# Performance work log

Hardware: AMD Instinct MI355X
Metric: run time of the kernel (lower is better)

The kernel has to match this reference:

```python
import jax, jax.numpy as jnp
from jax import lax
import numpy as np

L = 21                      # total_labels (incl. background class 0)
VARIANCES = (0.1, 0.1, 0.2, 0.2)
NMS_THRESHOLD = 0.5
MAX_TOTAL_SIZE = 200        # also max_output_size_per_class
SCORE_THRESHOLD = 0.5


def setup_inputs() -> dict:
    key = jax.random.key(0)
    k1, k2, k3, k4 = jax.random.split(key, 4)
    B, N = 1, 2048
    # valid normalized rois: y1<y2, x1<x2, inside [0,1]
    yx = jax.random.uniform(k1, (B, N, 2)) * 0.8
    hw = jax.random.uniform(k2, (B, N, 2)) * 0.19 + 0.01
    roi_bboxes = jnp.concatenate([yx, yx + hw], axis=-1)
    pred_deltas = jax.random.normal(k3, (B, N, L * 4)) * 0.2
    pred_label_probs = jax.random.uniform(k4, (B, N, L))
    return {"roi_bboxes": roi_bboxes, "pred_deltas": pred_deltas,
            "pred_label_probs": pred_label_probs}


def _decode(rois, deltas):
    # rois/deltas: (..., 4), boxes [y1,x1,y2,x2], deltas [dy,dx,dh,dw]
    h = rois[..., 2] - rois[..., 0]
    w = rois[..., 3] - rois[..., 1]
    cy = rois[..., 0] + 0.5 * h
    cx = rois[..., 1] + 0.5 * w
    nh = jnp.exp(deltas[..., 2]) * h
    nw = jnp.exp(deltas[..., 3]) * w
    ncy = deltas[..., 0] * h + cy
    ncx = deltas[..., 1] * w + cx
    return jnp.stack([ncy - 0.5 * nh, ncx - 0.5 * nw,
                      ncy + 0.5 * nh, ncx + 0.5 * nw], axis=-1)


def _iou_matrix(b):  # b: (N,4) -> (N,N)
    y1, x1, y2, x2 = b[:, 0], b[:, 1], b[:, 2], b[:, 3]
    area = (y2 - y1) * (x2 - x1)
    ih = jnp.clip(jnp.minimum(y2[:, None], y2[None, :]) - jnp.maximum(y1[:, None], y1[None, :]), 0.0)
    iw = jnp.clip(jnp.minimum(x2[:, None], x2[None, :]) - jnp.maximum(x1[:, None], x1[None, :]), 0.0)
    inter = ih * iw
    return inter / (area[:, None] + area[None, :] - inter + 1e-9)


def _nms_sorted(boxes, scores):
    # greedy per-class NMS; returns boxes/scores sorted by score desc + keep mask
    order = jnp.argsort(-scores)
    b = boxes[order]
    s = scores[order]
    iou = _iou_matrix(lax.stop_gradient(b))  # NMS decisions are non-differentiable
    n = b.shape[0]
    idx = jnp.arange(n)

    def body(i, keep):
        sup = keep[i] & (iou[i] > NMS_THRESHOLD) & (idx > i)
        return keep & jnp.logical_not(sup)

    keep = lax.fori_loop(0, n, body, jnp.ones((n,), bool))
    keep = keep & (jnp.cumsum(keep) <= MAX_TOTAL_SIZE)  # max_output_size_per_class
    return b, s, keep


def reference(roi_bboxes, pred_deltas, pred_label_probs):
    B, N, _ = roi_bboxes.shape  # B == 1 (module's slicing logic assumes it)
    deltas = pred_deltas.reshape(B, N, L, 4) * jnp.asarray(VARIANCES, pred_deltas.dtype)
    rois = jnp.broadcast_to(roi_bboxes[:, :, None, :], (B, N, L, 4))
    boxes = _decode(rois, deltas)  # (B,N,L,4)

    # zero out all class scores for rois whose argmax is background (class 0)
    am = jnp.argmax(pred_label_probs, axis=-1)
    scores = jnp.where((am != 0)[..., None], pred_label_probs, 0.0)

    boxes_c = jnp.transpose(boxes[0], (1, 0, 2))  # (L,N,4)
    scores_c = scores[0].T                         # (L,N)
    b_s, s_s, keep = jax.vmap(_nms_sorted)(boxes_c, scores_c)

    cls = jnp.broadcast_to(jnp.arange(L, dtype=s_s.dtype)[:, None], (L, N))
    flat_b = b_s.reshape(-1, 4)
    flat_s = s_s.reshape(-1)
    flat_c = cls.reshape(-1)

    def select(kmask):
        sc = jnp.where(kmask.reshape(-1), flat_s, -1.0)
        top_sc, top_idx = lax.top_k(sc, MAX_TOTAL_SIZE)
        return top_sc, jnp.clip(flat_b[top_idx], 0.0, 1.0), flat_c[top_idx]

    # thresholded combined NMS result (padded with zeros, like TF CNMS)
    sc_t, b_t, l_t = select(keep & (s_s > SCORE_THRESHOLD))
    valid_t = sc_t > SCORE_THRESHOLD
    out_b = jnp.where(valid_t[:, None], b_t, 0.0)
    out_s = jnp.where(valid_t, sc_t, 0.0)
    out_l = jnp.where(valid_t, l_t, 0.0)

    # fallback: no detections above threshold -> best unthresholded detection
    sc_u, b_u, l_u = select(keep)
    best = sc_u[0]
    have = best >= 0.001
    slot0 = jnp.arange(MAX_TOTAL_SIZE) == 0
    fb_b = jnp.where((slot0 & have)[:, None], b_u[0], 0.0)
    fb_s = jnp.where(slot0 & have, best, 0.0)
    fb_l = jnp.where(slot0 & have, l_u[0], 0.0)

    use_fb = jnp.sum(valid_t) == 0
    fin_b = jnp.where(use_fb, fb_b, out_b)[None]  # (1, MAX_TOTAL_SIZE, 4)
    fin_s = jnp.where(use_fb, fb_s, out_s)[None]  # (1, MAX_TOTAL_SIZE)
    fin_l = jnp.where(use_fb, fb_l, out_l)[None]  # (1, MAX_TOTAL_SIZE)
    return fin_b, fin_l, fin_s
```

## Files before the change

### kernel.cpp

```cpp
#include <hip/hip_runtime.h>
#include <stdint.h>

#define NN 2048
#define LL 21
#define CAP 200
#define TOT (LL * CAP)
#define TMAX 320
#define NCH (TMAX / 64)
#define NBK 1024
#define ARRCAP 1200

typedef unsigned long long u64;
typedef unsigned int u32;

__device__ __forceinline__ u64 shfl_u64(u64 v, int lane) {
    int lo = (int)(u32)(v & 0xFFFFFFFFull);
    int hi = (int)(u32)(v >> 32);
    lo = __shfl(lo, lane);
    hi = __shfl(hi, lane);
    return ((u64)(u32)hi << 32) | (u32)lo;
}

__device__ __forceinline__ u64 shfl_xor_u64(u64 v, int mask) {
    int lo = (int)(u32)(v & 0xFFFFFFFFull);
    int hi = (int)(u32)(v >> 32);
    lo = __shfl_xor(lo, mask);
    hi = __shfl_xor(hi, mask);
    return ((u64)(u32)hi << 32) | (u32)lo;
}

__device__ __forceinline__ float4 clip01(float4 b) {
    b.x = fminf(fmaxf(b.x, 0.0f), 1.0f);
    b.y = fminf(fmaxf(b.y, 0.0f), 1.0f);
    b.z = fminf(fmaxf(b.z, 0.0f), 1.0f);
    b.w = fminf(fmaxf(b.w, 0.0f), 1.0f);
    return b;
}

__device__ __forceinline__ float4 decode_box(const float4 roi, const float4 dd) {
#pragma clang fp contract(off)
    float h  = roi.z - roi.x;
    float w  = roi.w - roi.y;
    float cy = roi.x + 0.5f * h;
    float cx = roi.y + 0.5f * w;
    float d0 = dd.x * 0.1f;
    float d1 = dd.y * 0.1f;
    float d2 = dd.z * 0.2f;
    float d3 = dd.w * 0.2f;
    float nh = (float)exp((double)d2) * h;
    float nw = (float)exp((double)d3) * w;
    float ncy = d0 * h + cy;
    float ncx = d1 * w + cx;
    return make_float4(ncy - 0.5f * nh, ncx - 0.5f * nw, ncy + 0.5f * nh, ncx + 0.5f * nw);
}

__device__ __forceinline__ bool iou_gt(const float4 a, const float4 b) {
#pragma clang fp contract(off)
    float areaA = (a.z - a.x) * (a.w - a.y);
    float areaB = (b.z - b.x) * (b.w - b.y);
    float ih = fminf(a.z, b.z) - fmaxf(a.x, b.x);
    ih = fmaxf(ih, 0.0f);
    float iw = fminf(a.w, b.w) - fmaxf(a.y, b.y);
    iw = fmaxf(iw, 0.0f);
    float inter = ih * iw;
    float denom = ((areaA + areaB) - inter) + 1e-9f;
    return (inter / denom) > 0.5f;
}

__device__ __forceinline__ int rb_of(u64 key) {
    u32 sb = (u32)(key >> 32);
    int rb = 1023 - (int)((sb - 0x3F000000u) >> 13);
    return min(max(rb, 0), 1023);
}

__device__ __forceinline__ u64 lowmask(int n) {
    return (n >= 64) ? ~0ull : ((1ull << n) - 1ull);
}

__device__ __forceinline__ void desc_scan(int* histR, int* dstart, int* cursor,
                                          int* wtot, int t, int nthr) {
    const int PB = NBK / nthr;
    const int lane = t & 63, w = t >> 6;
    int c[4], local = 0;
    for (int k = 0; k < PB; ++k) { c[k] = histR[PB * t + k]; local += c[k]; }
    int incl = local;
    for (int d = 1; d < 64; d <<= 1) {
        int v = __shfl_up(incl, d);
        if (lane >= d) incl += v;
    }
    if (lane == 63) wtot[w] = incl;
    __syncthreads();
    int woff = 0;
    for (int i = 0; i < w; ++i) woff += wtot[i];
    int run = woff + incl - local;
    for (int k = 0; k < PB; ++k) {
        dstart[PB * t + k] = run;
        cursor[PB * t + k] = run;
        run += c[k];
    }
    __syncthreads();
}

__global__ __launch_bounds__(256) void score_kernel(
    const float* __restrict__ probs,
    u32* __restrict__ scoreT)
{
    __shared__ float tile[256 * LL];
    const int a0 = blockIdx.x * 256;
    const int t = threadIdx.x;
    const float4* src = (const float4*)probs + blockIdx.x * 1344;
    float4* dst = (float4*)tile;
    for (int i = t; i < 1344; i += 256) dst[i] = src[i];
    __syncthreads();
    const float* row = tile + t * LL;
    float best = row[0];
    int bi = 0;
    for (int j = 1; j < LL; ++j) {
        float v = row[j];
        if (v > best) { best = v; bi = j; }
    }
    for (int c = 0; c < LL; ++c)
        scoreT[c * NN + a0 + t] = (bi != 0) ? __float_as_uint(row[c]) : 0u;
}

#define SMEM_B 45056
#define NBASE 16384

__global__ __launch_bounds__(512) void per_class_kernel(
    const u32* __restrict__ scoreT,
    const float* __restrict__ roi,
    const float* __restrict__ deltas,
    u64* __restrict__ cand_key,
    float4* __restrict__ cand_box,
    u64* __restrict__ fb_key,
    float4* __restrict__ fb_box)
{
    const int cls = blockIdx.x;
    const int t = threadIdx.x;
    const int lane = t & 63;

    __shared__ char sm[SMEM_B];
    __shared__ int sCnt, sK;
    __shared__ u64 sGmax;
    __shared__ u64 keepm[NCH];
    __shared__ int wtot[8];

    u64* skey  = (u64*)sm;
    u64* skey3 = (u64*)sm;
    u64* skey2 = (u64*)(sm + NBASE);
    int* histR  = (int*)(sm + 32768);
    int* cursor = (int*)(sm + 36864);
    int* dstart = (int*)(sm + 40960);

    if (t == 0) { sCnt = 0; sK = 0; sGmax = 0ull; }
    for (int s = t; s < CAP; s += 512) cand_key[cls * CAP + s] = 0ull;
    for (int i = t; i < NBK; i += 512) histR[i] = 0;
    __syncthreads();

    uint4 s4 = ((const uint4*)(scoreT + cls * NN))[t];
    u32 sv[4] = { s4.x, s4.y, s4.z, s4.w };
    u64 lq[4];
    int ln = 0;
    u64 lmax = 0ull;
    for (int k = 0; k < 4; ++k) {
        u32 a = 4 * t + k;
        u64 key = ((u64)sv[k] << 32) | (u32)(~a);
        if (key > lmax) lmax = key;
        if (sv[k] > 0x3F000000u) lq[ln++] = key;
    }
    for (int d = 1; d < 64; d <<= 1) {
        u64 o = shfl_xor_u64(lmax, d);
        if (o > lmax) lmax = o;
    }
    if (lane == 0) atomicMax(&sGmax, lmax);
    int incl = ln;
    for (int d = 1; d < 64; d <<= 1) {
        int v = __shfl_up(incl, d);
        if (lane >= d) incl += v;
    }
    int wsum = __shfl(incl, 63);
    int wbase = 0;
    if (lane == 63) wbase = atomicAdd(&sCnt, wsum);
    wbase = __shfl(wbase, 63);
    int off = wbase + incl - ln;
    for (int j = 0; j < ln; ++j) skey[off + j] = lq[j];
    __syncthreads();
    const int M = sCnt;

    if (t == 0) {
        u64 g = sGmax;
        u32 a0 = ~(u32)(g & 0xFFFFFFFFull);
        float4 rb = *(const float4*)(roi + a0 * 4);
        float4 dd = *(const float4*)(deltas + a0 * (LL * 4) + cls * 4);
        fb_box[cls] = decode_box(rb, dd);
        fb_key[cls] = (g & 0xFFFFFFFF00000000ull) | (u32)(~(u32)(cls * NN));
    }

    for (int i = t; i < M; i += 512) atomicAdd(&histR[rb_of(skey[i])], 1);
    __syncthreads();
    desc_scan(histR, dstart, cursor, wtot, t, 512);
    for (int i = t; i < M; i += 512) {
        u64 k = skey[i];
        int pos = atomicAdd(&cursor[rb_of(k)], 1);
        skey2[pos] = k;
    }
    __syncthreads();
    for (int p = t; p < M; p += 512) {
        u64 k = skey2[p];
        int rb = rb_of(k);
        int s = dstart[rb], e = s + histR[rb];
        int rnk = s;
        for (int q = s; q < e; ++q) rnk += (skey2[q] > k) ? 1 : 0;
        skey3[rnk] = k;
    }
    __syncthreads();

    float4* cbox = (float4*)(sm + NBASE);
    u64* R  = (u64*)(sm + NBASE + 5120);
    u64* Tm = (u64*)(sm + NBASE + 7680);
    float4* kept = (float4*)(sm + NBASE + 12800);

    const int TT = min(M, TMAX);
    const int NCHe = (TT + 63) / 64;
    const int NJ = NCHe * (NCHe + 1) / 2;

    for (int r = t; r < TT; r += 512) {
        u32 a = ~(u32)(skey3[r] & 0xFFFFFFFFull);
        float4 rbx = *(const float4*)(roi + a * 4);
        float4 dd = *(const float4*)(deltas + a * (LL * 4) + cls * 4);
        cbox[r] = decode_box(rbx, dd);
    }
    __syncthreads();

    for (int task = t; task < NJ * 64; task += 512) {
        const int jobid = task >> 6, j = task & 63;
        int cj = 0, acc = 0;
        while (acc + cj + 1 <= jobid) { acc += cj + 1; ++cj; }
        const int ci = jobid - acc;
        const int gj = cj * 64 + j;
        const int nbj = min(64, TT - cj * 64);
        if (ci == cj) {
            u64 row = 0ull;
            if (j < nbj) {
                float4 bj = cbox[gj];
                for (int r2 = j + 1; r2 < nbj; ++r2)
                    if (iou_gt(bj, cbox[cj * 64 + r2])) row |= (1ull << r2);
            }
            R[cj * 64 + j] = row;
        } else {
            u64 wd = 0ull;
            if (j < nbj) {
                float4 bj = cbox[gj];
                const float4* cb = cbox + ci * 64;
                for (int i = 0; i < 64; ++i)
                    if (iou_gt(cb[i], bj)) wd |= (1ull << i);
            }
            Tm[(cj * (cj - 1) / 2 + ci) * 64 + j] = wd;
        }
    }
    __syncthreads();

    if (t < 64) {
        int K = 0;
        for (int cj = 0; cj < NCHe; ++cj) {
            if (K >= CAP) break;
            const int nb = min(64, TT - cj * 64);
            u64 row = R[cj * 64 + t];
            bool ext = (t >= nb);
            for (int ci = 0; ci < cj; ++ci)
                if (Tm[(cj * (cj - 1) / 2 + ci) * 64 + t] & keepm[ci]) ext = true;
            u64 rem = __ballot(ext);
            const u64 nz = __ballot(row != 0ull) & ~rem;
            u64 m = nz;
            while (m) {
                int i = __ffsll(m) - 1;
                u64 ri = shfl_u64(row, i);
                rem |= ri;
                u64 gt = (i == 63) ? 0ull : ~lowmask(i + 1);
                m = nz & ~rem & gt;
            }
            u64 keep = ~rem & lowmask(nb);
            if (t == 0) keepm[cj] = keep;
            if (t < nb && ((keep >> t) & 1ull)) {
                int krank = K + __popcll(keep & lowmask(t));
                if (krank < CAP) {
                    kept[krank] = cbox[cj * 64 + t];
                    int slot = cls * CAP + krank;
                    cand_key[slot] = (skey3[cj * 64 + t] & 0xFFFFFFFF00000000ull) |
                                     (u32)(~(u32)slot);
                    cand_box[slot] = cbox[cj * 64 + t];
                }
            }
            K += __popcll(keep);
        }
        if (t == 0) sK = K;
    }
    __syncthreads();

    int K = sK;
    if (K < CAP && M > TT) {
        u64* sup = (u64*)(sm + NBASE + 5120);
        unsigned char* extq = (unsigned char*)(sm + NBASE + 9216);
        const int g = t >> 6, r = t & 63;
        for (int base = TT; base < M; base += 64) {
            K = sK;
            if (K >= CAP) break;
            const int nb = min(64, M - base);
            if (t < nb) {
                u32 a = ~(u32)(skey3[base + t] & 0xFFFFFFFFull);
                float4 rbx = *(const float4*)(roi + a * 4);
                float4 dd = *(const float4*)(deltas + a * (LL * 4) + cls * 4);
                cbox[t] = decode_box(rbx, dd);
            }
            __syncthreads();
            u64 bits = 0ull;
            if (r < nb) {
                float4 br = cbox[r];
                int lo = max(r + 1, g * 8), hi = min(nb, (g + 1) * 8);
                for (int r2 = lo; r2 < hi; ++r2)
                    if (iou_gt(br, cbox[r2])) bits |= (1ull << r2);
            }
            sup[g * 64 + r] = bits;
            bool f = false;
            if (r < nb) {
                float4 bm = cbox[r];
                int per = (K + 7) >> 3;
                int e0 = g * per, e1 = min(K, e0 + per);
                for (int e = e0; e < e1; ++e)
                    if (iou_gt(kept[e], bm)) { f = true; break; }
            }
            extq[g * 64 + r] = f ? 1 : 0;
            __syncthreads();
            if (t < 64) {
                u64 row = 0ull;
                int extv = 0;
                for (int j = 0; j < 8; ++j) { row |= sup[j * 64 + t]; extv |= extq[j * 64 + t]; }
                bool ext = (t < nb) ? (extv != 0) : true;
                u64 rem = __ballot(ext);
                const u64 nz = __ballot(row != 0ull) & ~rem;
                u64 m = nz;
                while (m) {
                    int i = __ffsll(m) - 1;
                    u64 ri = shfl_u64(row, i);
                    rem |= ri;
                    u64 gt = (i == 63) ? 0ull : ~lowmask(i + 1);
                    m = nz & ~rem & gt;
                }
                u64 keep = ~rem & lowmask(nb);
                if (t < nb && ((keep >> t) & 1ull)) {
                    int krank = K + __popcll(keep & lowmask(t));
                    if (krank < CAP) {
                        kept[krank] = cbox[t];
                        int slot = cls * CAP + krank;
                        cand_key[slot] = (skey3[base + t] & 0xFFFFFFFF00000000ull) |
                                         (u32)(~(u32)slot);
                        cand_box[slot] = cbox[t];
                    }
                }
                if (t == 0) sK = K + __popcll(keep);
            }
            __syncthreads();
        }
    }
}

__global__ __launch_bounds__(256) void topk_kernel(
    const u64* __restrict__ cand_key,
    const float4* __restrict__ cand_box,
    const u64* __restrict__ fb_key,
    const float4* __restrict__ fb_box,
    float* __restrict__ out)
{
    const int t = threadIdx.x;
    __shared__ u64 keys[TOT];
    __shared__ int histR[NBK], cursor[NBK], dstart[NBK];
    __shared__ u64 arr[ARRCAP];
    __shared__ u64 outk[CAP];
    __shared__ int wtot[8];
    __shared__ int sRbstar;

    for (int i = t; i < NBK; i += 256) histR[i] = 0;
    for (int i = t; i < CAP; i += 256) outk[i] = 0ull;
    if (t == 0) sRbstar = NBK - 1;
    __syncthreads();

    const ulong2* ck2 = (const ulong2*)cand_key;
    for (int i = t; i < TOT / 2; i += 256) {
        ulong2 k2 = ck2[i];
        keys[2 * i]     = k2.x;
        keys[2 * i + 1] = k2.y;
        if (k2.x != 0ull) atomicAdd(&histR[rb_of(k2.x)], 1);
        if (k2.y != 0ull) atomicAdd(&histR[rb_of(k2.y)], 1);
    }
    __syncthreads();
    desc_scan(histR, dstart, cursor, wtot, t, 256);
    for (int k = 0; k < 4; ++k) {
        int rb = 4 * t + k;
        if (dstart[rb] < CAP && dstart[rb] + histR[rb] >= CAP) sRbstar = rb;
    }
    __syncthreads();
    const int rbstar = sRbstar;

    for (int i = t; i < TOT; i += 256) {
        u64 k = keys[i];
        if (k != 0ull) {
            int rb = rb_of(k);
            if (rb <= rbstar) {
                int pos = atomicAdd(&cursor[rb], 1);
                if (pos < ARRCAP) arr[pos] = k;
            }
        }
    }
    __syncthreads();

    const int E = min(dstart[rbstar] + histR[rbstar], ARRCAP);
    for (int p = t; p < E; p += 256) {
        u64 k = arr[p];
        int rb = rb_of(k);
        int s = dstart[rb], e = min(s + histR[rb], ARRCAP);
        int rnk = s;
        for (int q = s; q < e; ++q) rnk += (arr[q] > k) ? 1 : 0;
        if (rnk < CAP) outk[rnk] = k;
    }
    __syncthreads();

    for (int o = t; o < CAP; o += 256) {
        u64 key = outk[o];
        float4 b = make_float4(0.0f, 0.0f, 0.0f, 0.0f);
        float lab = 0.0f, sc = 0.0f;
        if (key != 0ull) {
            u32 slot = ~(u32)(key & 0xFFFFFFFFull);
            sc = __uint_as_float((u32)(key >> 32));
            lab = (float)(slot / CAP);
            b = clip01(cand_box[slot]);
        }
        out[o * 4 + 0] = b.x;
        out[o * 4 + 1] = b.y;
        out[o * 4 + 2] = b.z;
        out[o * 4 + 3] = b.w;
        out[4 * CAP + o] = lab;
        out[5 * CAP + o] = sc;
    }
    __syncthreads();

    if (t == 0 && outk[0] == 0ull) {
        u64 best = 0ull;
        int bc = 0;
        for (int c = 0; c < LL; ++c) {
            u64 k = fb_key[c];
            if (k > best) { best = k; bc = c; }
        }
        float bs = __uint_as_float((u32)(best >> 32));
        if (bs >= 0.001f) {
            float4 bb = clip01(fb_box[bc]);
            out[0] = bb.x; out[1] = bb.y; out[2] = bb.z; out[3] = bb.w;
            out[4 * CAP] = (float)bc;
            out[5 * CAP] = bs;
        }
    }
}

extern "C" void kernel_launch(void* const* d_in, const int* in_sizes, int n_in,
                              void* d_out, int out_size, void* d_ws, size_t ws_size,
                              hipStream_t stream) {
    const float* roi    = (const float*)d_in[0];
    const float* deltas = (const float*)d_in[1];
    const float* probs  = (const float*)d_in[2];
    float* out = (float*)d_out;

    char* ws = (char*)d_ws;
    u32*    scoreT   = (u32*)ws;
    u64*    cand_key = (u64*)(ws + 172032);
    float4* cand_box = (float4*)(ws + 205632);
    u64*    fb_key   = (u64*)(ws + 272832);
    float4* fb_box   = (float4*)(ws + 273008);

    score_kernel<<<NN / 256, 256, 0, stream>>>(probs, scoreT);
    per_class_kernel<<<LL, 512, 0, stream>>>(scoreT, roi, deltas,
                                             cand_key, cand_box, fb_key, fb_box);
    topk_kernel<<<1, 256, 0, stream>>>(cand_key, cand_box, fb_key, fb_box, out);
}
```

Measured before the change: 93.66 us.

## Fuse top-k into per-class kernel via last-block counter and precompute box areas

Drops the separate top-k launch: each per-class block increments a global counter once it finishes, and the last block to finish runs the cross-class top-k merge using 512 threads. The change also folds the histogram build into the key scatter and decodes candidate boxes inside the rank loop, removing two barriers. Box areas are computed once and stored in shared memory so the IoU loops do not recompute them. In exchange it adds a memset launch, atomics and fences, and more shared memory per block. The merge work is now serialised behind the slowest class block.

```diff
diff --git a/kernel.cpp b/kernel.cpp
--- a/kernel.cpp
+++ b/kernel.cpp
@@ -54,6 +54,11 @@
     return make_float4(ncy - 0.5f * nh, ncx - 0.5f * nw, ncy + 0.5f * nh, ncx + 0.5f * nw);
 }
 
+__device__ __forceinline__ float area_of(const float4 b) {
+#pragma clang fp contract(off)
+    return (b.z - b.x) * (b.w - b.y);
+}
+
 __device__ __forceinline__ bool iou_gt(const float4 a, const float4 b) {
 #pragma clang fp contract(off)
     float areaA = (a.z - a.x) * (a.w - a.y);
@@ -67,6 +72,18 @@
     return (inter / denom) > 0.5f;
 }
 
+__device__ __forceinline__ bool iou_gt_pre(const float4 a, const float4 b,
+                                           float areaA, float areaB) {
+#pragma clang fp contract(off)
+    float ih = fminf(a.z, b.z) - fmaxf(a.x, b.x);
+    ih = fmaxf(ih, 0.0f);
+    float iw = fminf(a.w, b.w) - fmaxf(a.y, b.y);
+    iw = fmaxf(iw, 0.0f);
+    float inter = ih * iw;
+    float denom = ((areaA + areaB) - inter) + 1e-9f;
+    return (inter / denom) > 0.5f;
+}
+
 __device__ __forceinline__ int rb_of(u64 key) {
     u32 sb = (u32)(key >> 32);
     int rb = 1023 - (int)((sb - 0x3F000000u) >> 13);
@@ -123,8 +140,11 @@
         scoreT[c * NN + a0 + t] = (bi != 0) ? __float_as_uint(row[c]) : 0u;
 }
 
-#define SMEM_B 45056
-#define NBASE 16384
+#define SMEM_B 64384
+#define A1OFF 17408
+#define A2OFF 34816
+#define A3OFF 47104
+#define A4OFF 63104
 
 __global__ __launch_bounds__(512) void per_class_kernel(
     const u32* __restrict__ scoreT,
@@ -133,24 +153,31 @@
     u64* __restrict__ cand_key,
     float4* __restrict__ cand_box,
     u64* __restrict__ fb_key,
-    float4* __restrict__ fb_box)
+    float4* __restrict__ fb_box,
+    int* __restrict__ ctr,
+    float* __restrict__ out)
 {
     const int cls = blockIdx.x;
     const int t = threadIdx.x;
     const int lane = t & 63;
 
     __shared__ char sm[SMEM_B];
-    __shared__ int sCnt, sK;
+    __shared__ int sCnt, sK, sLast, sRbstar;
     __shared__ u64 sGmax;
     __shared__ u64 keepm[NCH];
     __shared__ int wtot[8];
 
     u64* skey  = (u64*)sm;
     u64* skey3 = (u64*)sm;
-    u64* skey2 = (u64*)(sm + NBASE);
-    int* histR  = (int*)(sm + 32768);
-    int* cursor = (int*)(sm + 36864);
-    int* dstart = (int*)(sm + 40960);
+    u64* skey2 = (u64*)(sm + A1OFF);
+    int* histR  = (int*)(sm + A2OFF);
+    int* cursor = (int*)(sm + A2OFF + 4096);
+    int* dstart = (int*)(sm + A2OFF + 8192);
+    float4* cbox = (float4*)(sm + A3OFF);
+    u64* R  = (u64*)(sm + A3OFF + 5120);
+    u64* Tm = (u64*)(sm + A3OFF + 7680);
+    float4* kept = (float4*)(sm + A3OFF + 12800);
+    float* area = (float*)(sm + A4OFF);
 
     if (t == 0) { sCnt = 0; sK = 0; sGmax = 0ull; }
     for (int s = t; s < CAP; s += 512) cand_key[cls * CAP + s] = 0ull;
@@ -183,9 +210,13 @@
     if (lane == 63) wbase = atomicAdd(&sCnt, wsum);
     wbase = __shfl(wbase, 63);
     int off = wbase + incl - ln;
-    for (int j = 0; j < ln; ++j) skey[off + j] = lq[j];
+    for (int j = 0; j < ln; ++j) {
+        skey[off + j] = lq[j];
+        atomicAdd(&histR[rb_of(lq[j])], 1);
+    }
     __syncthreads();
     const int M = sCnt;
+    const int TT = min(M, TMAX);
 
     if (t == 0) {
         u64 g = sGmax;
@@ -196,15 +227,15 @@
         fb_key[cls] = (g & 0xFFFFFFFF00000000ull) | (u32)(~(u32)(cls * NN));
     }
 
-    for (int i = t; i < M; i += 512) atomicAdd(&histR[rb_of(skey[i])], 1);
-    __syncthreads();
     desc_scan(histR, dstart, cursor, wtot, t, 512);
+
     for (int i = t; i < M; i += 512) {
         u64 k = skey[i];
         int pos = atomicAdd(&cursor[rb_of(k)], 1);
         skey2[pos] = k;
     }
     __syncthreads();
+
     for (int p = t; p < M; p += 512) {
         u64 k = skey2[p];
         int rb = rb_of(k);
@@ -212,25 +243,19 @@
         int rnk = s;
         for (int q = s; q < e; ++q) rnk += (skey2[q] > k) ? 1 : 0;
         skey3[rnk] = k;
-    }
-    __syncthreads();
-
-    float4* cbox = (float4*)(sm + NBASE);
-    u64* R  = (u64*)(sm + NBASE + 5120);
-    u64* Tm = (u64*)(sm + NBASE + 7680);
-    float4* kept = (float4*)(sm + NBASE + 12800);
-
-    const int TT = min(M, TMAX);
+        if (rnk < TT) {
+            u32 a = ~(u32)(k & 0xFFFFFFFFull);
+            float4 rbx = *(const float4*)(roi + a * 4);
+            float4 dd = *(const float4*)(deltas + a * (LL * 4) + cls * 4);
+            float4 bx = decode_box(rbx, dd);
+            cbox[rnk] = bx;
+            area[rnk] = area_of(bx);
+        }
+    }
+    __syncthreads();
+
     const int NCHe = (TT + 63) / 64;
     const int NJ = NCHe * (NCHe + 1) / 2;
-
-    for (int r = t; r < TT; r += 512) {
-        u32 a = ~(u32)(skey3[r] & 0xFFFFFFFFull);
-        float4 rbx = *(const float4*)(roi + a * 4);
-        float4 dd = *(const float4*)(deltas + a * (LL * 4) + cls * 4);
-        cbox[r] = decode_box(rbx, dd);
-    }
-    __syncthreads();
 
     for (int task = t; task < NJ * 64; task += 512) {
         const int jobid = task >> 6, j = task & 63;
@@ -243,17 +268,21 @@
             u64 row = 0ull;
             if (j < nbj) {
                 float4 bj = cbox[gj];
+                float aj = area[gj];
                 for (int r2 = j + 1; r2 < nbj; ++r2)
-                    if (iou_gt(bj, cbox[cj * 64 + r2])) row |= (1ull << r2);
+                    if (iou_gt_pre(bj, cbox[cj * 64 + r2], aj, area[cj * 64 + r2]))
+                        row |= (1ull << r2);
             }
             R[cj * 64 + j] = row;
         } else {
             u64 wd = 0ull;
             if (j < nbj) {
                 float4 bj = cbox[gj];
+                float aj = area[gj];
                 const float4* cb = cbox + ci * 64;
+                const float* ca = area + ci * 64;
                 for (int i = 0; i < 64; ++i)
-                    if (iou_gt(cb[i], bj)) wd |= (1ull << i);
+                    if (iou_gt_pre(cb[i], bj, ca[i], aj)) wd |= (1ull << i);
             }
             Tm[(cj * (cj - 1) / 2 + ci) * 64 + j] = wd;
         }
@@ -299,8 +328,8 @@
 
     int K = sK;
     if (K < CAP && M > TT) {
-        u64* sup = (u64*)(sm + NBASE + 5120);
-        unsigned char* extq = (unsigned char*)(sm + NBASE + 9216);
+        u64* sup = (u64*)(sm + A3OFF + 5120);
+        unsigned char* extq = (unsigned char*)(sm + A3OFF + 9216);
         const int g = t >> 6, r = t & 63;
         for (int base = TT; base < M; base += 64) {
             K = sK;
@@ -362,100 +391,109 @@
             __syncthreads();
         }
     }
-}
-
-__global__ __launch_bounds__(256) void topk_kernel(
-    const u64* __restrict__ cand_key,
-    const float4* __restrict__ cand_box,
-    const u64* __restrict__ fb_key,
-    const float4* __restrict__ fb_box,
-    float* __restrict__ out)
-{
-    const int t = threadIdx.x;
-    __shared__ u64 keys[TOT];
-    __shared__ int histR[NBK], cursor[NBK], dstart[NBK];
-    __shared__ u64 arr[ARRCAP];
-    __shared__ u64 outk[CAP];
-    __shared__ int wtot[8];
-    __shared__ int sRbstar;
-
-    for (int i = t; i < NBK; i += 256) histR[i] = 0;
-    for (int i = t; i < CAP; i += 256) outk[i] = 0ull;
-    if (t == 0) sRbstar = NBK - 1;
-    __syncthreads();
-
-    const ulong2* ck2 = (const ulong2*)cand_key;
-    for (int i = t; i < TOT / 2; i += 256) {
-        ulong2 k2 = ck2[i];
-        keys[2 * i]     = k2.x;
-        keys[2 * i + 1] = k2.y;
-        if (k2.x != 0ull) atomicAdd(&histR[rb_of(k2.x)], 1);
-        if (k2.y != 0ull) atomicAdd(&histR[rb_of(k2.y)], 1);
-    }
-    __syncthreads();
-    desc_scan(histR, dstart, cursor, wtot, t, 256);
-    for (int k = 0; k < 4; ++k) {
-        int rb = 4 * t + k;
-        if (dstart[rb] < CAP && dstart[rb] + histR[rb] >= CAP) sRbstar = rb;
-    }
-    __syncthreads();
-    const int rbstar = sRbstar;
-
-    for (int i = t; i < TOT; i += 256) {
-        u64 k = keys[i];
-        if (k != 0ull) {
+
+    __threadfence();
+    if (t == 0) {
+        int old = __hip_atomic_fetch_add(ctr, 1, __ATOMIC_ACQ_REL, __HIP_MEMORY_SCOPE_AGENT);
+        sLast = (old == LL - 1) ? 1 : 0;
+        sRbstar = NBK - 1;
+    }
+    __syncthreads();
+    if (!sLast) return;
+
+    {
+        u64* keys = (u64*)sm;
+        u64* arr  = (u64*)(sm + A3OFF);
+        u64* outk = (u64*)(sm + A3OFF + 9600);
+
+        for (int i = t; i < NBK; i += 512) histR[i] = 0;
+        for (int i = t; i < CAP; i += 512) outk[i] = 0ull;
+        __syncthreads();
+
+        for (int i = t; i < TOT; i += 512) {
+            u64 k = __hip_atomic_load(&cand_key[i], __ATOMIC_RELAXED,
+                                      __HIP_MEMORY_SCOPE_AGENT);
+            keys[i] = k;
+            if (k != 0ull) atomicAdd(&histR[rb_of(k)], 1);
+        }
+        __syncthreads();
+        desc_scan(histR, dstart, cursor, wtot, t, 512);
+        for (int k = 0; k < 2; ++k) {
+            int rb = 2 * t + k;
+            if (dstart[rb] < CAP && dstart[rb] + histR[rb] >= CAP) sRbstar = rb;
+        }
+        __syncthreads();
+        const int rbstar = sRbstar;
+
+        for (int i = t; i < TOT; i += 512) {
+            u64 k = keys[i];
+            if (k != 0ull) {
+                int rb = rb_of(k);
+                if (rb <= rbstar) {
+                    int pos = atomicAdd(&cursor[rb], 1);
+                    if (pos < ARRCAP) arr[pos] = k;
+                }
+            }
+        }
+        __syncthreads();
+
+        const int E = min(dstart[rbstar] + histR[rbstar], ARRCAP);
+        for (int p = t; p < E; p += 512) {
+            u64 k = arr[p];
             int rb = rb_of(k);
-            if (rb <= rbstar) {
-                int pos = atomicAdd(&cursor[rb], 1);
-                if (pos < ARRCAP) arr[pos] = k;
-            }
-        }
-    }
-    __syncthreads();
-
-    const int E = min(dstart[rbstar] + histR[rbstar], ARRCAP);
-    for (int p = t; p < E; p += 256) {
-        u64 k = arr[p];
-        int rb = rb_of(k);
-        int s = dstart[rb], e = min(s + histR[rb], ARRCAP);
-        int rnk = s;
-        for (int q = s; q < e; ++q) rnk += (arr[q] > k) ? 1 : 0;
-        if (rnk < CAP) outk[rnk] = k;
-    }
-    __syncthreads();
-
-    for (int o = t; o < CAP; o += 256) {
-        u64 key = outk[o];
-        float4 b = make_float4(0.0f, 0.0f, 0.0f, 0.0f);
-        float lab = 0.0f, sc = 0.0f;
-        if (key != 0ull) {
-            u32 slot = ~(u32)(key & 0xFFFFFFFFull);
-            sc = __uint_as_float((u32)(key >> 32));
-            lab = (float)(slot / CAP);
-            b = clip01(cand_box[slot]);
-        }
-        out[o * 4 + 0] = b.x;
-        out[o * 4 + 1] = b.y;
-        out[o * 4 + 2] = b.z;
-        out[o * 4 + 3] = b.w;
-        out[4 * CAP + o] = lab;
-        out[5 * CAP + o] = sc;
-    }
-    __syncthreads();
-
-    if (t == 0 && outk[0] == 0ull) {
-        u64 best = 0ull;
-        int bc = 0;
-        for (int c = 0; c < LL; ++c) {
-            u64 k = fb_key[c];
-            if (k > best) { best = k; bc = c; }
-        }
-        float bs = __uint_as_float((u32)(best >> 32));
-        if (bs >= 0.001f) {
-            float4 bb = clip01(fb_box[bc]);
-            out[0] = bb.x; out[1] = bb.y; out[2] = bb.z; out[3] = bb.w;
-            out[4 * CAP] = (float)bc;
-            out[5 * CAP] = bs;
+            int s = dstart[rb], e = min(s + histR[rb], ARRCAP);
+            int rnk = s;
+            for (int q = s; q < e; ++q) rnk += (arr[q] > k) ? 1 : 0;
+            if (rnk < CAP) outk[rnk] = k;
+        }
+        __syncthreads();
+
+        for (int o = t; o < CAP; o += 512) {
+            u64 key = outk[o];
+            float4 b = make_float4(0.0f, 0.0f, 0.0f, 0.0f);
+            float lab = 0.0f, sc = 0.0f;
+            if (key != 0ull) {
+                u32 slot = ~(u32)(key & 0xFFFFFFFFull);
+                sc = __uint_as_float((u32)(key >> 32));
+                lab = (float)(slot / CAP);
+                const u64* bp = (const u64*)&cand_box[slot];
+                u64 w0 = __hip_atomic_load(bp,     __ATOMIC_RELAXED, __HIP_MEMORY_SCOPE_AGENT);
+                u64 w1 = __hip_atomic_load(bp + 1, __ATOMIC_RELAXED, __HIP_MEMORY_SCOPE_AGENT);
+                float4 bb;
+                ((u64*)&bb)[0] = w0;
+                ((u64*)&bb)[1] = w1;
+                b = clip01(bb);
+            }
+            out[o * 4 + 0] = b.x;
+            out[o * 4 + 1] = b.y;
+            out[o * 4 + 2] = b.z;
+            out[o * 4 + 3] = b.w;
+            out[4 * CAP + o] = lab;
+            out[5 * CAP + o] = sc;
+        }
+        __syncthreads();
+
+        if (t == 0 && outk[0] == 0ull) {
+            u64 best = 0ull;
+            int bc = 0;
+            for (int c = 0; c < LL; ++c) {
+                u64 k = __hip_atomic_load(&fb_key[c], __ATOMIC_RELAXED,
+                                          __HIP_MEMORY_SCOPE_AGENT);
+                if (k > best) { best = k; bc = c; }
+            }
+            float bs = __uint_as_float((u32)(best >> 32));
+            if (bs >= 0.001f) {
+                const u64* bp = (const u64*)&fb_box[bc];
+                u64 w0 = __hip_atomic_load(bp,     __ATOMIC_RELAXED, __HIP_MEMORY_SCOPE_AGENT);
+                u64 w1 = __hip_atomic_load(bp + 1, __ATOMIC_RELAXED, __HIP_MEMORY_SCOPE_AGENT);
+                float4 bb;
+                ((u64*)&bb)[0] = w0;
+                ((u64*)&bb)[1] = w1;
+                bb = clip01(bb);
+                out[0] = bb.x; out[1] = bb.y; out[2] = bb.z; out[3] = bb.w;
+                out[4 * CAP] = (float)bc;
+                out[5 * CAP] = bs;
+            }
         }
     }
 }
@@ -474,9 +512,11 @@
     float4* cand_box = (float4*)(ws + 205632);
     u64*    fb_key   = (u64*)(ws + 272832);
     float4* fb_box   = (float4*)(ws + 273008);
-
+    int*    ctr      = (int*)(ws + 273344);
+
+    (void)hipMemsetAsync(ctr, 0, 4, stream);
     score_kernel<<<NN / 256, 256, 0, stream>>>(probs, scoreT);
     per_class_kernel<<<LL, 512, 0, stream>>>(scoreT, roi, deltas,
-                                             cand_key, cand_box, fb_key, fb_box);
-    topk_kernel<<<1, 256, 0, stream>>>(cand_key, cand_box, fb_key, fb_box, out);
-}
+                                             cand_key, cand_box, fb_key, fb_box,
+                                             ctr, out);
+}
```

Result: no change. 94.93 us (+1.4%).
